# Kernel optimization log

Hardware: AMD Instinct MI355X
Metric: run time of the kernel (lower is better)

Reference implementation:

```python
import jax, jax.numpy as jnp
import numpy as np

B, N, F, D, C = 4096, 8, 64, 64, 10  # batch, carriages, phys dim, bond dim, output classes


def setup_inputs() -> dict:
    key = jax.random.key(0)
    k1, k2, k3, k4 = jax.random.split(key, 4)
    scale = 1.0 / np.sqrt(F * D)
    x = jax.random.normal(k1, (B, N, F), dtype=jnp.float32)
    core_first = jax.random.normal(k2, (C, F, D), dtype=jnp.float32) * scale  # A1: (left=1 squeezed, up=C, p=F, right=D)
    cores_mid = jax.random.normal(k3, (N - 2, D, F, D), dtype=jnp.float32) * scale  # A2..A7: (D, up=1 squeezed, F, D)
    core_last = jax.random.normal(k4, (D, F), dtype=jnp.float32) * scale  # A8: (D, up=1, F, right=1 squeezed)
    return {"x": x, "core_first": core_first, "cores_mid": cores_mid, "core_last": core_last}


def reference(x, core_first, cores_mid, core_last):
    # Tensor-train forward: out[s, c] = sum over bond chain of
    #   A1[c, p1, r1] x[s,0,p1] * prod_i A_i[l, p_i, r] x[s,i,p_i] * A_N[l, p_N] x[s,N-1,p_N]
    # First carriage: contract physical leg -> (B, C, D)
    T0 = jnp.einsum('sp,cpr->scr', x[:, 0], core_first)
    # Middle carriages: sequential chain of small bond-dim GEMMs via scan
    xs_mid = jnp.moveaxis(x[:, 1:-1], 1, 0)  # (N-2, B, F)

    def step(T, inp):
        xi, core = inp  # xi: (B, F), core: (D, F, D)
        M = jnp.einsum('sp,lpr->slr', xi, core)  # (B, D, D)
        return jnp.einsum('scl,slr->scr', T, M), None

    T, _ = jax.lax.scan(step, T0, (xs_mid, cores_mid))
    # Last carriage: contract physical and close the chain -> (B, C)
    m_last = jnp.einsum('sp,lp->sl', x[:, -1], core_last)  # (B, D)
    out = jnp.einsum('scl,sl->sc', T, m_last)
    return out
```

## Files before the change

### kernel.cpp

```cpp
#include <hip/hip_runtime.h>


typedef _Float16 half8 __attribute__((ext_vector_type(8)));
typedef _Float16 half4 __attribute__((ext_vector_type(4)));
typedef float f32x4 __attribute__((ext_vector_type(4)));

#define LAST_OFF   0
#define MID_OFF    4096
#define MID_SZ     262144
#define FIRST_OFF  1576960
#define N_FRAGS    3208

__global__ __launch_bounds__(256) void tt_swz(
    const float* __restrict__ cf,
    const float* __restrict__ cm,
    const float* __restrict__ cl,
    _Float16* __restrict__ ws)
{
  int gid = blockIdx.x * 256 + threadIdx.x;
  if (gid >= N_FRAGS * 64) return;
  int lane = gid & 63, frag = gid >> 6;
  int quad = lane >> 4, m16 = lane & 15;
  half8 hv;
  _Float16* dst;
  if (frag < 8) {
    int t = frag >> 1, kt = frag & 1;
    int l = t * 16 + m16;
    const float* s = cl + l * 64 + kt * 32 + quad * 8;
#pragma unroll
    for (int j = 0; j < 8; ++j) hv[j] = (_Float16)s[j];
    dst = ws + LAST_OFF + (size_t)((t * 2 + kt) * 64 + lane) * 8;
  } else if (frag < 8 + 3072) {
    int f2 = frag - 8;
    int ci = f2 >> 9, rem = f2 & 511;
    int t = rem >> 1, kt = rem & 1;
    int l = (t & 3) * 16 + m16, p = t >> 2;
    const float* s = cm + (((size_t)ci * 64 + l) * 64 + p) * 64 + kt * 32 + quad * 8;
#pragma unroll
    for (int j = 0; j < 8; ++j) hv[j] = (_Float16)s[j];
    dst = ws + MID_OFF + (size_t)ci * MID_SZ + (size_t)(rem * 64 + lane) * 8;
  } else {
    int f2 = frag - 3080;
    int t = f2 >> 1, kt = f2 & 1;
    int c = m16, p = t;
    if (c < 10) {
      const float* s = cf + ((size_t)(c * 64 + p)) * 64 + kt * 32 + quad * 8;
#pragma unroll
      for (int j = 0; j < 8; ++j) hv[j] = (_Float16)s[j];
    } else {
#pragma unroll
      for (int j = 0; j < 8; ++j) hv[j] = (_Float16)0.f;
    }
    dst = ws + FIRST_OFF + (size_t)((t * 2 + kt) * 64 + lane) * 8;
  }
  *(half8*)dst = hv;
}

__global__ __launch_bounds__(512) void tt_main(
    const float* __restrict__ x,
    const _Float16* __restrict__ ws,
    float* __restrict__ out)
{
  __shared__ __align__(16) float Xs[512 * 17];
  __shared__ __align__(16) _Float16 Vt[2][16][72];
  __shared__ __align__(16) float Red[8][16][16];
  const int tid = threadIdx.x;
  const int w = tid >> 6, lane = tid & 63;
  const int quad = lane >> 4, sl = lane & 15;
  const int blk = blockIdx.x;

  {
    const float* xb = x + (size_t)blk * 16 * 512;
    int s = tid & 15, b0 = (tid >> 4) * 4;
#pragma unroll
    for (int k = 0; k < 4; ++k) {
      int base = b0 + k * 128;
      float4 v = *(const float4*)(xb + s * 512 + base);
      Xs[(base + 0) * 17 + s] = v.x;
      Xs[(base + 1) * 17 + s] = v.y;
      Xs[(base + 2) * 17 + s] = v.z;
      Xs[(base + 3) * 17 + s] = v.w;
    }
  }
  __syncthreads();

  {
    int kt = w >> 2, tt = w & 3;
    half8 b;
#pragma unroll
    for (int j = 0; j < 8; ++j)
      b[j] = (_Float16)Xs[(448 + kt * 32 + quad * 8 + j) * 17 + sl];
    half8 a = *(const half8*)(ws + LAST_OFF + (size_t)((tt * 2 + kt) * 64 + lane) * 8);
    f32x4 d = {0.f, 0.f, 0.f, 0.f};
    d = __builtin_amdgcn_mfma_f32_16x16x32_f16(a, b, d, 0, 0, 0);
    half4 hv;
#pragma unroll
    for (int r = 0; r < 4; ++r) hv[r] = (_Float16)d[r];
    *(half4*)&Vt[kt][sl][tt * 16 + quad * 4] = hv;
  }
  __syncthreads();

  const int h = w >> 2, g = w & 3;
  for (int step = 0; step < 6; ++step) {
    int ci = 5 - step;
    const _Float16* base = ws + MID_OFF + (size_t)ci * MID_SZ;
    half8 b0 = *(const half8*)&Vt[0][sl][quad * 8];
    half8 b0p = *(const half8*)&Vt[1][sl][quad * 8];
    half8 b1 = *(const half8*)&Vt[0][sl][32 + quad * 8];
    half8 b1p = *(const half8*)&Vt[1][sl][32 + quad * 8];
    b0 = b0 + b0p; b1 = b1 + b1p;
    __syncthreads();
    float a0c = 0.f, a1c = 0.f, a2c = 0.f, a3c = 0.f;
    const int xrow = (ci + 1) * 64;
#pragma unroll 8
    for (int j = 0; j < 32; ++j) {
      int t = 8 * j + w;
      int p = t >> 2;
      const _Float16* fp = base + (size_t)t * 1024 + (size_t)lane * 8;
      half8 A0 = *(const half8*)fp;
      half8 A1 = *(const half8*)(fp + 512);
      f32x4 dd = {0.f, 0.f, 0.f, 0.f};
      dd = __builtin_amdgcn_mfma_f32_16x16x32_f16(A0, b0, dd, 0, 0, 0);
      dd = __builtin_amdgcn_mfma_f32_16x16x32_f16(A1, b1, dd, 0, 0, 0);
      float xv = Xs[(xrow + p) * 17 + sl];
      a0c += xv * dd[0]; a1c += xv * dd[1];
      a2c += xv * dd[2]; a3c += xv * dd[3];
    }
    half4 hv;
    hv[0] = (_Float16)a0c; hv[1] = (_Float16)a1c;
    hv[2] = (_Float16)a2c; hv[3] = (_Float16)a3c;
    *(half4*)&Vt[h][sl][g * 16 + quad * 4] = hv;
    __syncthreads();
  }

  {
    half8 b0 = *(const half8*)&Vt[0][sl][quad * 8];
    half8 b0p = *(const half8*)&Vt[1][sl][quad * 8];
    half8 b1 = *(const half8*)&Vt[0][sl][32 + quad * 8];
    half8 b1p = *(const half8*)&Vt[1][sl][32 + quad * 8];
    b0 = b0 + b0p; b1 = b1 + b1p;
    float f0 = 0.f, f1 = 0.f, f2 = 0.f, f3 = 0.f;
#pragma unroll
    for (int j = 0; j < 8; ++j) {
      int t = 8 * j + w;
      const _Float16* fp = ws + FIRST_OFF + (size_t)t * 1024 + (size_t)lane * 8;
      half8 A0 = *(const half8*)fp;
      half8 A1 = *(const half8*)(fp + 512);
      f32x4 dd = {0.f, 0.f, 0.f, 0.f};
      dd = __builtin_amdgcn_mfma_f32_16x16x32_f16(A0, b0, dd, 0, 0, 0);
      dd = __builtin_amdgcn_mfma_f32_16x16x32_f16(A1, b1, dd, 0, 0, 0);
      float xv = Xs[t * 17 + sl];
      f0 += xv * dd[0]; f1 += xv * dd[1];
      f2 += xv * dd[2]; f3 += xv * dd[3];
    }
    Red[w][quad * 4 + 0][sl] = f0;
    Red[w][quad * 4 + 1][sl] = f1;
    Red[w][quad * 4 + 2][sl] = f2;
    Red[w][quad * 4 + 3][sl] = f3;
  }
  __syncthreads();
  if (tid < 256) {
    int c = tid >> 4, s = tid & 15;
    float sum = 0.f;
#pragma unroll
    for (int ww = 0; ww < 8; ++ww) sum += Red[ww][c][s];
    if (c < 10) out[((size_t)blk * 16 + s) * 10 + c] = sum;
  }
}

extern "C" void kernel_launch(void* const* d_in, const int* in_sizes, int n_in,
                              void* d_out, int out_size, void* d_ws, size_t ws_size,
                              hipStream_t stream) {
  const float* x  = (const float*)d_in[0];
  const float* cf = (const float*)d_in[1];
  const float* cm = (const float*)d_in[2];
  const float* cl = (const float*)d_in[3];
  _Float16* ws = (_Float16*)d_ws;
  float* out = (float*)d_out;
  tt_swz<<<dim3((N_FRAGS * 64 + 255) / 256), dim3(256), 0, stream>>>(cf, cm, cl, ws);
  tt_main<<<dim3(256), dim3(512), 0, stream>>>(x, ws, out);
}
```

Measured before the change: 102.1 us.

## Process 32 samples per block with 1024 threads, reusing core fragments across two sample tiles

```diff
diff --git a/kernel.cpp b/kernel.cpp
--- a/kernel.cpp
+++ b/kernel.cpp
@@ -3,6 +3,7 @@
 
 typedef _Float16 half8 __attribute__((ext_vector_type(8)));
 typedef _Float16 half4 __attribute__((ext_vector_type(4)));
+typedef _Float16 half2v __attribute__((ext_vector_type(2)));
 typedef float f32x4 __attribute__((ext_vector_type(4)));
 
 #define LAST_OFF   0
@@ -56,115 +57,156 @@
   *(half8*)dst = hv;
 }
 
-__global__ __launch_bounds__(512) void tt_main(
+__global__ __launch_bounds__(1024) void tt_main(
     const float* __restrict__ x,
     const _Float16* __restrict__ ws,
     float* __restrict__ out)
 {
-  __shared__ __align__(16) float Xs[512 * 17];
-  __shared__ __align__(16) _Float16 Vt[2][16][72];
-  __shared__ __align__(16) float Red[8][16][16];
+  __shared__ __align__(16) _Float16 Xs[512][33];
+  __shared__ __align__(16) _Float16 Vt[4][32][72];
+  __shared__ __align__(16) _Float16 Vc[32][72];
   const int tid = threadIdx.x;
   const int w = tid >> 6, lane = tid & 63;
   const int quad = lane >> 4, sl = lane & 15;
   const int blk = blockIdx.x;
 
   {
-    const float* xb = x + (size_t)blk * 16 * 512;
-    int s = tid & 15, b0 = (tid >> 4) * 4;
+    const float* xb = x + (size_t)blk * 32 * 512;
+    int s = tid >> 5, q = tid & 31;
 #pragma unroll
     for (int k = 0; k < 4; ++k) {
-      int base = b0 + k * 128;
-      float4 v = *(const float4*)(xb + s * 512 + base);
-      Xs[(base + 0) * 17 + s] = v.x;
-      Xs[(base + 1) * 17 + s] = v.y;
-      Xs[(base + 2) * 17 + s] = v.z;
-      Xs[(base + 3) * 17 + s] = v.w;
-    }
+      int f4 = q + 32 * k;
+      float4 v = *(const float4*)(xb + (size_t)s * 512 + (size_t)f4 * 4);
+      int row = f4 * 4;
+      Xs[row + 0][s] = (_Float16)v.x;
+      Xs[row + 1][s] = (_Float16)v.y;
+      Xs[row + 2][s] = (_Float16)v.z;
+      Xs[row + 3][s] = (_Float16)v.w;
+    }
+    _Float16* vz = &Vt[2][0][0];
+    for (int idx = tid; idx < 2 * 32 * 72; idx += 1024) vz[idx] = (_Float16)0.f;
   }
   __syncthreads();
 
   {
-    int kt = w >> 2, tt = w & 3;
+    int st = w >> 3, kt = (w >> 2) & 1, tt = w & 3;
     half8 b;
 #pragma unroll
     for (int j = 0; j < 8; ++j)
-      b[j] = (_Float16)Xs[(448 + kt * 32 + quad * 8 + j) * 17 + sl];
+      b[j] = Xs[448 + kt * 32 + quad * 8 + j][st * 16 + sl];
     half8 a = *(const half8*)(ws + LAST_OFF + (size_t)((tt * 2 + kt) * 64 + lane) * 8);
     f32x4 d = {0.f, 0.f, 0.f, 0.f};
     d = __builtin_amdgcn_mfma_f32_16x16x32_f16(a, b, d, 0, 0, 0);
     half4 hv;
 #pragma unroll
     for (int r = 0; r < 4; ++r) hv[r] = (_Float16)d[r];
-    *(half4*)&Vt[kt][sl][tt * 16 + quad * 4] = hv;
-  }
-  __syncthreads();
-
-  const int h = w >> 2, g = w & 3;
+    *(half4*)&Vt[kt][st * 16 + sl][tt * 16 + quad * 4] = hv;
+  }
+  __syncthreads();
+  {
+    int s = tid >> 5, rp = tid & 31;
+    float r0 = 0.f, r1 = 0.f;
+#pragma unroll
+    for (int p = 0; p < 4; ++p) {
+      half2v h = *(const half2v*)&Vt[p][s][rp * 2];
+      r0 += (float)h[0]; r1 += (float)h[1];
+    }
+    half2v o; o[0] = (_Float16)r0; o[1] = (_Float16)r1;
+    *(half2v*)&Vc[s][rp * 2] = o;
+  }
+  __syncthreads();
+
+  const int g = w & 3, part = w >> 2;
   for (int step = 0; step < 6; ++step) {
     int ci = 5 - step;
-    const _Float16* base = ws + MID_OFF + (size_t)ci * MID_SZ;
-    half8 b0 = *(const half8*)&Vt[0][sl][quad * 8];
-    half8 b0p = *(const half8*)&Vt[1][sl][quad * 8];
-    half8 b1 = *(const half8*)&Vt[0][sl][32 + quad * 8];
-    half8 b1p = *(const half8*)&Vt[1][sl][32 + quad * 8];
-    b0 = b0 + b0p; b1 = b1 + b1p;
-    __syncthreads();
-    float a0c = 0.f, a1c = 0.f, a2c = 0.f, a3c = 0.f;
+    half8 b00 = *(const half8*)&Vc[sl][quad * 8];
+    half8 b01 = *(const half8*)&Vc[sl][32 + quad * 8];
+    half8 b10 = *(const half8*)&Vc[16 + sl][quad * 8];
+    half8 b11 = *(const half8*)&Vc[16 + sl][32 + quad * 8];
+    const _Float16* wl = ws + MID_OFF + (size_t)ci * MID_SZ
+                       + (size_t)w * 1024 + (size_t)lane * 8;
+    float c00 = 0.f, c01 = 0.f, c02 = 0.f, c03 = 0.f;
+    float c10 = 0.f, c11 = 0.f, c12 = 0.f, c13 = 0.f;
     const int xrow = (ci + 1) * 64;
-#pragma unroll 8
-    for (int j = 0; j < 32; ++j) {
-      int t = 8 * j + w;
+#pragma unroll 4
+    for (int j = 0; j < 16; ++j) {
+      int t = j * 16 + w;
       int p = t >> 2;
-      const _Float16* fp = base + (size_t)t * 1024 + (size_t)lane * 8;
+      const _Float16* fp = wl + (size_t)j * 16384;
       half8 A0 = *(const half8*)fp;
       half8 A1 = *(const half8*)(fp + 512);
-      f32x4 dd = {0.f, 0.f, 0.f, 0.f};
-      dd = __builtin_amdgcn_mfma_f32_16x16x32_f16(A0, b0, dd, 0, 0, 0);
-      dd = __builtin_amdgcn_mfma_f32_16x16x32_f16(A1, b1, dd, 0, 0, 0);
-      float xv = Xs[(xrow + p) * 17 + sl];
-      a0c += xv * dd[0]; a1c += xv * dd[1];
-      a2c += xv * dd[2]; a3c += xv * dd[3];
-    }
-    half4 hv;
-    hv[0] = (_Float16)a0c; hv[1] = (_Float16)a1c;
-    hv[2] = (_Float16)a2c; hv[3] = (_Float16)a3c;
-    *(half4*)&Vt[h][sl][g * 16 + quad * 4] = hv;
+      f32x4 d0 = {0.f, 0.f, 0.f, 0.f}, d1 = {0.f, 0.f, 0.f, 0.f};
+      d0 = __builtin_amdgcn_mfma_f32_16x16x32_f16(A0, b00, d0, 0, 0, 0);
+      d0 = __builtin_amdgcn_mfma_f32_16x16x32_f16(A1, b01, d0, 0, 0, 0);
+      d1 = __builtin_amdgcn_mfma_f32_16x16x32_f16(A0, b10, d1, 0, 0, 0);
+      d1 = __builtin_amdgcn_mfma_f32_16x16x32_f16(A1, b11, d1, 0, 0, 0);
+      float xv0 = (float)Xs[xrow + p][sl];
+      float xv1 = (float)Xs[xrow + p][16 + sl];
+      c00 += xv0 * d0[0]; c01 += xv0 * d0[1]; c02 += xv0 * d0[2]; c03 += xv0 * d0[3];
+      c10 += xv1 * d1[0]; c11 += xv1 * d1[1]; c12 += xv1 * d1[2]; c13 += xv1 * d1[3];
+    }
+    half4 h0, h1;
+    h0[0] = (_Float16)c00; h0[1] = (_Float16)c01; h0[2] = (_Float16)c02; h0[3] = (_Float16)c03;
+    h1[0] = (_Float16)c10; h1[1] = (_Float16)c11; h1[2] = (_Float16)c12; h1[3] = (_Float16)c13;
+    *(half4*)&Vt[part][sl][g * 16 + quad * 4] = h0;
+    *(half4*)&Vt[part][16 + sl][g * 16 + quad * 4] = h1;
     __syncthreads();
-  }
-
-  {
-    half8 b0 = *(const half8*)&Vt[0][sl][quad * 8];
-    half8 b0p = *(const half8*)&Vt[1][sl][quad * 8];
-    half8 b1 = *(const half8*)&Vt[0][sl][32 + quad * 8];
-    half8 b1p = *(const half8*)&Vt[1][sl][32 + quad * 8];
-    b0 = b0 + b0p; b1 = b1 + b1p;
-    float f0 = 0.f, f1 = 0.f, f2 = 0.f, f3 = 0.f;
+    {
+      int s = tid >> 5, rp = tid & 31;
+      float r0 = 0.f, r1 = 0.f;
+#pragma unroll
+      for (int p = 0; p < 4; ++p) {
+        half2v h = *(const half2v*)&Vt[p][s][rp * 2];
+        r0 += (float)h[0]; r1 += (float)h[1];
+      }
+      half2v o; o[0] = (_Float16)r0; o[1] = (_Float16)r1;
+      *(half2v*)&Vc[s][rp * 2] = o;
+    }
+    __syncthreads();
+  }
+
+  float* Red = (float*)&Vt[0][0][0];
+  if (w < 8) {
+    half8 b00 = *(const half8*)&Vc[sl][quad * 8];
+    half8 b01 = *(const half8*)&Vc[sl][32 + quad * 8];
+    half8 b10 = *(const half8*)&Vc[16 + sl][quad * 8];
+    half8 b11 = *(const half8*)&Vc[16 + sl][32 + quad * 8];
+    float f00 = 0.f, f01 = 0.f, f02 = 0.f, f03 = 0.f;
+    float f10 = 0.f, f11 = 0.f, f12 = 0.f, f13 = 0.f;
 #pragma unroll
     for (int j = 0; j < 8; ++j) {
-      int t = 8 * j + w;
+      int t = j * 8 + w;
       const _Float16* fp = ws + FIRST_OFF + (size_t)t * 1024 + (size_t)lane * 8;
       half8 A0 = *(const half8*)fp;
       half8 A1 = *(const half8*)(fp + 512);
-      f32x4 dd = {0.f, 0.f, 0.f, 0.f};
-      dd = __builtin_amdgcn_mfma_f32_16x16x32_f16(A0, b0, dd, 0, 0, 0);
-      dd = __builtin_amdgcn_mfma_f32_16x16x32_f16(A1, b1, dd, 0, 0, 0);
-      float xv = Xs[t * 17 + sl];
-      f0 += xv * dd[0]; f1 += xv * dd[1];
-      f2 += xv * dd[2]; f3 += xv * dd[3];
-    }
-    Red[w][quad * 4 + 0][sl] = f0;
-    Red[w][quad * 4 + 1][sl] = f1;
-    Red[w][quad * 4 + 2][sl] = f2;
-    Red[w][quad * 4 + 3][sl] = f3;
-  }
-  __syncthreads();
-  if (tid < 256) {
-    int c = tid >> 4, s = tid & 15;
+      f32x4 d0 = {0.f, 0.f, 0.f, 0.f}, d1 = {0.f, 0.f, 0.f, 0.f};
+      d0 = __builtin_amdgcn_mfma_f32_16x16x32_f16(A0, b00, d0, 0, 0, 0);
+      d0 = __builtin_amdgcn_mfma_f32_16x16x32_f16(A1, b01, d0, 0, 0, 0);
+      d1 = __builtin_amdgcn_mfma_f32_16x16x32_f16(A0, b10, d1, 0, 0, 0);
+      d1 = __builtin_amdgcn_mfma_f32_16x16x32_f16(A1, b11, d1, 0, 0, 0);
+      float xv0 = (float)Xs[t][sl];
+      float xv1 = (float)Xs[t][16 + sl];
+      f00 += xv0 * d0[0]; f01 += xv0 * d0[1]; f02 += xv0 * d0[2]; f03 += xv0 * d0[3];
+      f10 += xv1 * d1[0]; f11 += xv1 * d1[1]; f12 += xv1 * d1[2]; f13 += xv1 * d1[3];
+    }
+    float a0[4] = {f00, f01, f02, f03};
+    float a1[4] = {f10, f11, f12, f13};
+#pragma unroll
+    for (int r = 0; r < 4; ++r) {
+      int c = quad * 4 + r;
+      if (c < 10) {
+        Red[(w * 10 + c) * 32 + sl] = a0[r];
+        Red[(w * 10 + c) * 32 + 16 + sl] = a1[r];
+      }
+    }
+  }
+  __syncthreads();
+  if (tid < 320) {
+    int c = tid >> 5, s = tid & 31;
     float sum = 0.f;
 #pragma unroll
-    for (int ww = 0; ww < 8; ++ww) sum += Red[ww][c][s];
-    if (c < 10) out[((size_t)blk * 16 + s) * 10 + c] = sum;
+    for (int ww = 0; ww < 8; ++ww) sum += Red[(ww * 10 + c) * 32 + s];
+    out[((size_t)blk * 32 + s) * 10 + c] = sum;
   }
 }
 
@@ -178,5 +220,5 @@
   _Float16* ws = (_Float16*)d_ws;
   float* out = (float*)d_out;
   tt_swz<<<dim3((N_FRAGS * 64 + 255) / 256), dim3(256), 0, stream>>>(cf, cm, cl, ws);
-  tt_main<<<dim3(256), dim3(512), 0, stream>>>(x, ws, out);
+  tt_main<<<dim3(128), dim3(1024), 0, stream>>>(x, ws, out);
 }
```

After: 101.6 us. No clear change (-0.5%).

## Double block size to 16 waves, splitting mid-chain K reduction four ways

Applied to the files above, without the earlier changes.

```diff
diff --git a/kernel.cpp b/kernel.cpp
--- a/kernel.cpp
+++ b/kernel.cpp
@@ -56,14 +56,14 @@
   *(half8*)dst = hv;
 }
 
-__global__ __launch_bounds__(512) void tt_main(
+__global__ __launch_bounds__(1024) void tt_main(
     const float* __restrict__ x,
     const _Float16* __restrict__ ws,
     float* __restrict__ out)
 {
   __shared__ __align__(16) float Xs[512 * 17];
-  __shared__ __align__(16) _Float16 Vt[2][16][72];
-  __shared__ __align__(16) float Red[8][16][16];
+  __shared__ __align__(16) _Float16 Vt[4][16][72];
+  __shared__ __align__(16) float Red[16][16][16];
   const int tid = threadIdx.x;
   const int w = tid >> 6, lane = tid & 63;
   const int quad = lane >> 4, sl = lane & 15;
@@ -73,18 +73,20 @@
     const float* xb = x + (size_t)blk * 16 * 512;
     int s = tid & 15, b0 = (tid >> 4) * 4;
 #pragma unroll
-    for (int k = 0; k < 4; ++k) {
-      int base = b0 + k * 128;
+    for (int k = 0; k < 2; ++k) {
+      int base = b0 + k * 256;
       float4 v = *(const float4*)(xb + s * 512 + base);
       Xs[(base + 0) * 17 + s] = v.x;
       Xs[(base + 1) * 17 + s] = v.y;
       Xs[(base + 2) * 17 + s] = v.z;
       Xs[(base + 3) * 17 + s] = v.w;
     }
+    _Float16* vz = &Vt[2][0][0];
+    for (int idx = tid; idx < 2 * 16 * 72; idx += 1024) vz[idx] = (_Float16)0.f;
   }
   __syncthreads();
 
-  {
+  if (w < 8) {
     int kt = w >> 2, tt = w & 3;
     half8 b;
 #pragma unroll
@@ -100,49 +102,59 @@
   }
   __syncthreads();
 
-  const int h = w >> 2, g = w & 3;
+  const int pq = w >> 2;
+  const int lch = (w & 3) * 16;
   for (int step = 0; step < 6; ++step) {
     int ci = 5 - step;
     const _Float16* base = ws + MID_OFF + (size_t)ci * MID_SZ;
     half8 b0 = *(const half8*)&Vt[0][sl][quad * 8];
-    half8 b0p = *(const half8*)&Vt[1][sl][quad * 8];
+    half8 b0b = *(const half8*)&Vt[1][sl][quad * 8];
+    half8 b0c = *(const half8*)&Vt[2][sl][quad * 8];
+    half8 b0d = *(const half8*)&Vt[3][sl][quad * 8];
     half8 b1 = *(const half8*)&Vt[0][sl][32 + quad * 8];
-    half8 b1p = *(const half8*)&Vt[1][sl][32 + quad * 8];
-    b0 = b0 + b0p; b1 = b1 + b1p;
+    half8 b1b = *(const half8*)&Vt[1][sl][32 + quad * 8];
+    half8 b1c = *(const half8*)&Vt[2][sl][32 + quad * 8];
+    half8 b1d = *(const half8*)&Vt[3][sl][32 + quad * 8];
+    b0 = (b0 + b0b) + (b0c + b0d);
+    b1 = (b1 + b1b) + (b1c + b1d);
     __syncthreads();
-    float a0c = 0.f, a1c = 0.f, a2c = 0.f, a3c = 0.f;
+    float a0 = 0.f, a1 = 0.f, a2 = 0.f, a3 = 0.f;
     const int xrow = (ci + 1) * 64;
-#pragma unroll 8
-    for (int j = 0; j < 32; ++j) {
-      int t = 8 * j + w;
-      int p = t >> 2;
+#pragma unroll
+    for (int j = 0; j < 16; ++j) {
+      int t = 16 * j + w;
       const _Float16* fp = base + (size_t)t * 1024 + (size_t)lane * 8;
       half8 A0 = *(const half8*)fp;
       half8 A1 = *(const half8*)(fp + 512);
       f32x4 dd = {0.f, 0.f, 0.f, 0.f};
       dd = __builtin_amdgcn_mfma_f32_16x16x32_f16(A0, b0, dd, 0, 0, 0);
       dd = __builtin_amdgcn_mfma_f32_16x16x32_f16(A1, b1, dd, 0, 0, 0);
-      float xv = Xs[(xrow + p) * 17 + sl];
-      a0c += xv * dd[0]; a1c += xv * dd[1];
-      a2c += xv * dd[2]; a3c += xv * dd[3];
+      float xv = Xs[(xrow + 4 * j + pq) * 17 + sl];
+      a0 += xv * dd[0]; a1 += xv * dd[1];
+      a2 += xv * dd[2]; a3 += xv * dd[3];
     }
     half4 hv;
-    hv[0] = (_Float16)a0c; hv[1] = (_Float16)a1c;
-    hv[2] = (_Float16)a2c; hv[3] = (_Float16)a3c;
-    *(half4*)&Vt[h][sl][g * 16 + quad * 4] = hv;
+    hv[0] = (_Float16)a0; hv[1] = (_Float16)a1;
+    hv[2] = (_Float16)a2; hv[3] = (_Float16)a3;
+    *(half4*)&Vt[pq][sl][lch + quad * 4] = hv;
     __syncthreads();
   }
 
   {
     half8 b0 = *(const half8*)&Vt[0][sl][quad * 8];
-    half8 b0p = *(const half8*)&Vt[1][sl][quad * 8];
+    half8 b0b = *(const half8*)&Vt[1][sl][quad * 8];
+    half8 b0c = *(const half8*)&Vt[2][sl][quad * 8];
+    half8 b0d = *(const half8*)&Vt[3][sl][quad * 8];
     half8 b1 = *(const half8*)&Vt[0][sl][32 + quad * 8];
-    half8 b1p = *(const half8*)&Vt[1][sl][32 + quad * 8];
-    b0 = b0 + b0p; b1 = b1 + b1p;
+    half8 b1b = *(const half8*)&Vt[1][sl][32 + quad * 8];
+    half8 b1c = *(const half8*)&Vt[2][sl][32 + quad * 8];
+    half8 b1d = *(const half8*)&Vt[3][sl][32 + quad * 8];
+    b0 = (b0 + b0b) + (b0c + b0d);
+    b1 = (b1 + b1b) + (b1c + b1d);
     float f0 = 0.f, f1 = 0.f, f2 = 0.f, f3 = 0.f;
 #pragma unroll
-    for (int j = 0; j < 8; ++j) {
-      int t = 8 * j + w;
+    for (int j = 0; j < 4; ++j) {
+      int t = 16 * j + w;
       const _Float16* fp = ws + FIRST_OFF + (size_t)t * 1024 + (size_t)lane * 8;
       half8 A0 = *(const half8*)fp;
       half8 A1 = *(const half8*)(fp + 512);
@@ -161,10 +173,12 @@
   __syncthreads();
   if (tid < 256) {
     int c = tid >> 4, s = tid & 15;
-    float sum = 0.f;
+    if (c < 10) {
+      float sum = 0.f;
 #pragma unroll
-    for (int ww = 0; ww < 8; ++ww) sum += Red[ww][c][s];
-    if (c < 10) out[((size_t)blk * 16 + s) * 10 + c] = sum;
+      for (int ww = 0; ww < 16; ++ww) sum += Red[ww][c][s];
+      out[((size_t)blk * 16 + s) * 10 + c] = sum;
+    }
   }
 }
 
@@ -178,5 +192,5 @@
   _Float16* ws = (_Float16*)d_ws;
   float* out = (float*)d_out;
   tt_swz<<<dim3((N_FRAGS * 64 + 255) / 256), dim3(256), 0, stream>>>(cf, cm, cl, ws);
-  tt_main<<<dim3(256), dim3(512), 0, stream>>>(x, ws, out);
+  tt_main<<<dim3(256), dim3(1024), 0, stream>>>(x, ws, out);
 }
```

Result: slower. 107.7 us (+5.5%).
